# Performance work log

Hardware: AMD Instinct MI355X
Metric: run time of the kernel (lower is better)

## Reference

```python
import jax, jax.numpy as jnp
import numpy as np

N_ATOMS = 200000
AEV_DIM = 384
H1, H2, H3 = 160, 128, 96
N_SPECIES = 4
ALPHA = 0.1  # CELU alpha used by ANI atomic networks


def setup_inputs() -> dict:
    key = jax.random.key(0)
    ks = jax.random.split(key, 8)
    aev = jax.random.normal(ks[0], (N_ATOMS, AEV_DIM), dtype=jnp.float32)
    # Disjoint species partition (matches (species==s).nonzero() buffers)
    perm = jax.random.permutation(ks[1], N_ATOMS)
    chunk = N_ATOMS // N_SPECIES
    H_idx = perm[0 * chunk:1 * chunk]
    C_idx = perm[1 * chunk:2 * chunk]
    N_idx = perm[2 * chunk:3 * chunk]
    O_idx = perm[3 * chunk:4 * chunk]

    def init(k, shape, fan_in):
        return (jax.random.normal(k, shape, dtype=jnp.float32) / np.float32(np.sqrt(fan_in)))

    # Stacked per-species MLP params: leading axis = species (H,C,N,O)
    W1 = init(ks[2], (N_SPECIES, AEV_DIM, H1), AEV_DIM); b1 = jnp.zeros((N_SPECIES, H1), jnp.float32)
    W2 = init(ks[3], (N_SPECIES, H1, H2), H1);          b2 = jnp.zeros((N_SPECIES, H2), jnp.float32)
    W3 = init(ks[4], (N_SPECIES, H2, H3), H2);          b3 = jnp.zeros((N_SPECIES, H3), jnp.float32)
    W4 = init(ks[5], (N_SPECIES, H3, 1), H3);           b4 = jnp.zeros((N_SPECIES, 1), jnp.float32)
    return {"aev": aev,
            "W1": W1, "b1": b1, "W2": W2, "b2": b2,
            "W3": W3, "b3": b3, "W4": W4, "b4": b4,
            "H_idx": H_idx, "C_idx": C_idx, "N_idx": N_idx, "O_idx": O_idx}


def _species_mlp(x, W1, b1, W2, b2, W3, b3, W4, b4):
    h = jax.nn.celu(x @ W1 + b1, ALPHA)
    h = jax.nn.celu(h @ W2 + b2, ALPHA)
    h = jax.nn.celu(h @ W3 + b3, ALPHA)
    return (h @ W4 + b4).reshape(-1)  # per-atom scalar energy


def reference(aev, W1, b1, W2, b2, W3, b3, W4, b4, H_idx, C_idx, N_idx, O_idx):
    out = jnp.zeros((aev.shape[0],), dtype=aev.dtype)
    # Fixed small loop over the 4 species networks (structurally distinct experts)
    for s, idx in enumerate((H_idx, C_idx, N_idx, O_idx)):
        e = _species_mlp(aev[idx], W1[s], b1[s], W2[s], b2[s], W3[s], b3[s], W4[s], b4[s])
        out = out.at[idx].add(e)  # index_add_ scatter
    # output.unsqueeze(0).sum(dim=1) -> molecular energy, shape [1]
    return out[None, :].sum(axis=1)
```

## Files before the change

### kernel.cpp

```cpp
#include <hip/hip_runtime.h>

#define DI __device__ __forceinline__

constexpr int AEV = 384;
constexpr int H1N = 160;
constexpr int H2N = 128;
constexpr int H3N = 96;
constexpr int NSP = 4;
constexpr int W1P = 200;
constexpr int W2P = 168;
constexpr int W3P = 136;
constexpr int W3OFF = H2N * W2P;

using half8  = __attribute__((ext_vector_type(8))) _Float16;
using half4v = __attribute__((ext_vector_type(4))) _Float16;
using f32x4  = __attribute__((ext_vector_type(4))) float;

__device__ __align__(16) _Float16 g_w1[NSP * H1N * AEV];
__device__ __align__(16) _Float16 g_w2[NSP * H2N * H1N];
__device__ __align__(16) _Float16 g_w3[NSP * H3N * H2N];

DI float celu_f(float x) {
  return fmaxf(x, 0.f) + 0.1f * (exp2f(fminf(x, 0.f) * 14.426950408889634f) - 1.f);
}
DI f32x4 mfma16h(half8 a, half8 b, f32x4 c) {
  return __builtin_amdgcn_mfma_f32_16x16x32_f16(a, b, c, 0, 0, 0);
}
DI half8 cvt8(float4 a, float4 b) {
  half8 t;
  t[0] = (_Float16)a.x; t[1] = (_Float16)a.y; t[2] = (_Float16)a.z; t[3] = (_Float16)a.w;
  t[4] = (_Float16)b.x; t[5] = (_Float16)b.y; t[6] = (_Float16)b.z; t[7] = (_Float16)b.w;
  return t;
}
DI half4v shfl4(half4v v, int src) {
  union { half4v h; int i[2]; } u;
  u.h = v;
  u.i[0] = __shfl(u.i[0], src, 64);
  u.i[1] = __shfl(u.i[1], src, 64);
  return u.h;
}
DI half8 bfrag(const half4v* hb, int ks, int l15, int quad) {
  const int sLo = (quad & 1) * 32 + l15, sHi = sLo + 16;
  half4v loA = shfl4(hb[2 * ks], sLo),     loB = shfl4(hb[2 * ks + 1], sLo);
  half4v hiA = shfl4(hb[2 * ks], sHi),     hiB = shfl4(hb[2 * ks + 1], sHi);
  half4v lo = (quad & 2) ? loB : loA;
  half4v hi = (quad & 2) ? hiB : hiA;
  half8 b;
  b[0] = lo[0]; b[1] = lo[1]; b[2] = lo[2]; b[3] = lo[3];
  b[4] = hi[0]; b[5] = hi[1]; b[6] = hi[2]; b[7] = hi[3];
  return b;
}

template <int K, int N>
DI void tp(const float* __restrict__ src, _Float16* dst, int id) {
  constexpr int per = K * N;
  int s = id / per, r = id % per;
  int n = r / K, k = r % K;
  dst[s * per + n * K + k] = (_Float16)src[s * per + k * N + n];
}

__global__ void prep(const float* __restrict__ W1, const float* __restrict__ W2,
                     const float* __restrict__ W3, float* __restrict__ out) {
  int id = blockIdx.x * 256 + threadIdx.x;
  if (id == 0) out[0] = 0.f;
  constexpr int E1 = NSP * AEV * H1N;
  constexpr int E2 = NSP * H1N * H2N;
  constexpr int E3 = NSP * H2N * H3N;
  if (id < E1)                 tp<AEV, H1N>(W1, g_w1, id);
  else if (id < E1 + E2)       tp<H1N, H2N>(W2, g_w2, id - E1);
  else if (id < E1 + E2 + E3)  tp<H2N, H3N>(W3, g_w3, id - E1 - E2);
}

__global__ __launch_bounds__(512, 4) void fused_mlp(
    const float* __restrict__ aev,
    const float* __restrict__ b1, const float* __restrict__ b2,
    const float* __restrict__ b3,
    const float* __restrict__ W4, const float* __restrict__ pb4,
    const int* __restrict__ i0, const int* __restrict__ i1,
    const int* __restrict__ i2, const int* __restrict__ i3,
    int chunk, float* __restrict__ out) {
  __shared__ __align__(16) _Float16 WS[34560];
  __shared__ float RED[8];

  const int tid  = threadIdx.x;
  const int lane = tid & 63, wav = tid >> 6;
  const int l15  = lane & 15, quad = lane >> 4;
  const int s    = blockIdx.y;
  const int* idx = (s == 0) ? i0 : (s == 1) ? i1 : (s == 2) ? i2 : i3;

  const int a = blockIdx.x * 128 + wav * 16 + l15;
  const bool valid = (a < chunk);
  const int r = idx[valid ? a : (chunk - 1)];
  const float* xr = aev + (size_t)r * AEV + quad * 8;

  const _Float16* w1src = g_w1 + (size_t)s * H1N * AEV;

#pragma unroll
  for (int i = 0; i < 8; ++i) {
    int c = tid + i * 512;
    if (c < H1N * 24) {
      int n = c / 24, kc = c % 24;
      *(half8*)(WS + n * W1P + kc * 8) = *(const half8*)(w1src + n * AEV + kc * 8);
    }
  }
  __syncthreads();

  f32x4 acc[10];
#pragma unroll
  for (int m = 0; m < 10; ++m)
#pragma unroll
    for (int i = 0; i < 4; ++i) acc[m][i] = 0.f;

  float4 xf0 = *(const float4*)(xr), xf1 = *(const float4*)(xr + 4);
#pragma unroll
  for (int ks = 0; ks < 6; ++ks) {
    half8 bv = cvt8(xf0, xf1);
    xf0 = *(const float4*)(xr + (ks + 1) * 32);
    xf1 = *(const float4*)(xr + (ks + 1) * 32 + 4);
#pragma unroll
    for (int mt = 0; mt < 10; ++mt) {
      half8 aw = *(const half8*)(WS + (mt * 16 + l15) * W1P + ks * 32 + quad * 8);
      acc[mt] = mfma16h(aw, bv, acc[mt]);
    }
  }
  __syncthreads();
#pragma unroll
  for (int i = 0; i < 8; ++i) {
    int c = tid + i * 512;
    if (c < H1N * 24) {
      int n = c / 24, kc = c % 24;
      *(half8*)(WS + n * W1P + kc * 8) = *(const half8*)(w1src + 192 + n * AEV + kc * 8);
    }
  }
  __syncthreads();
#pragma unroll
  for (int ks = 6; ks < 12; ++ks) {
    half8 bv = cvt8(xf0, xf1);
    if (ks < 11) {
      xf0 = *(const float4*)(xr + (ks + 1) * 32);
      xf1 = *(const float4*)(xr + (ks + 1) * 32 + 4);
    }
#pragma unroll
    for (int mt = 0; mt < 10; ++mt) {
      half8 aw = *(const half8*)(WS + (mt * 16 + l15) * W1P + (ks - 6) * 32 + quad * 8);
      acc[mt] = mfma16h(aw, bv, acc[mt]);
    }
  }
  half4v hb[10];
#pragma unroll
  for (int mt = 0; mt < 10; ++mt) {
    float4 bb = *(const float4*)(b1 + s * H1N + mt * 16 + quad * 4);
    half4v o;
    o[0] = (_Float16)celu_f(acc[mt][0] + bb.x);
    o[1] = (_Float16)celu_f(acc[mt][1] + bb.y);
    o[2] = (_Float16)celu_f(acc[mt][2] + bb.z);
    o[3] = (_Float16)celu_f(acc[mt][3] + bb.w);
    hb[mt] = o;
  }

  __syncthreads();
  {
    const _Float16* w2src = g_w2 + (size_t)s * H2N * H1N;
    const _Float16* w3src = g_w3 + (size_t)s * H3N * H2N;
#pragma unroll
    for (int i = 0; i < 5; ++i) {
      int c = tid + i * 512;
      int n = c / 20, kc = c % 20;
      *(half8*)(WS + n * W2P + kc * 8) = *(const half8*)(w2src + n * H1N + kc * 8);
    }
#pragma unroll
    for (int i = 0; i < 3; ++i) {
      int c = tid + i * 512;
      int n = c / 16, kc = c % 16;
      *(half8*)(WS + W3OFF + n * W3P + kc * 8) = *(const half8*)(w3src + n * H2N + kc * 8);
    }
  }
  __syncthreads();

  f32x4 acc2[8];
#pragma unroll
  for (int m = 0; m < 8; ++m)
#pragma unroll
    for (int i = 0; i < 4; ++i) acc2[m][i] = 0.f;
#pragma unroll
  for (int ks = 0; ks < 5; ++ks) {
    half8 bv = bfrag(hb, ks, l15, quad);
#pragma unroll
    for (int mt = 0; mt < 8; ++mt) {
      half8 aw = *(const half8*)(WS + (mt * 16 + l15) * W2P + ks * 32 + quad * 8);
      acc2[mt] = mfma16h(aw, bv, acc2[mt]);
    }
  }
  half4v hb2[8];
#pragma unroll
  for (int mt = 0; mt < 8; ++mt) {
    float4 bb = *(const float4*)(b2 + s * H2N + mt * 16 + quad * 4);
    half4v o;
    o[0] = (_Float16)celu_f(acc2[mt][0] + bb.x);
    o[1] = (_Float16)celu_f(acc2[mt][1] + bb.y);
    o[2] = (_Float16)celu_f(acc2[mt][2] + bb.z);
    o[3] = (_Float16)celu_f(acc2[mt][3] + bb.w);
    hb2[mt] = o;
  }

  f32x4 acc3[6];
#pragma unroll
  for (int m = 0; m < 6; ++m)
#pragma unroll
    for (int i = 0; i < 4; ++i) acc3[m][i] = 0.f;
#pragma unroll
  for (int ks = 0; ks < 4; ++ks) {
    half8 bv = bfrag(hb2, ks, l15, quad);
#pragma unroll
    for (int mt = 0; mt < 6; ++mt) {
      half8 aw = *(const half8*)(WS + W3OFF + (mt * 16 + l15) * W3P + ks * 32 + quad * 8);
      acc3[mt] = mfma16h(aw, bv, acc3[mt]);
    }
  }

  float e = 0.f;
#pragma unroll
  for (int mt = 0; mt < 6; ++mt) {
    float4 bb = *(const float4*)(b3 + s * H3N + mt * 16 + quad * 4);
    float4 wv = *(const float4*)(W4 + s * H3N + mt * 16 + quad * 4);
    e += (float)(_Float16)celu_f(acc3[mt][0] + bb.x) * wv.x
       + (float)(_Float16)celu_f(acc3[mt][1] + bb.y) * wv.y
       + (float)(_Float16)celu_f(acc3[mt][2] + bb.z) * wv.z
       + (float)(_Float16)celu_f(acc3[mt][3] + bb.w) * wv.w;
  }
  e += __shfl_xor(e, 16, 64);
  e += __shfl_xor(e, 32, 64);
  e = (lane < 16 && valid) ? (e + pb4[s]) : 0.f;
#pragma unroll
  for (int off = 1; off < 64; off <<= 1) e += __shfl_xor(e, off, 64);
  if (lane == 0) RED[wav] = e;
  __syncthreads();
  if (tid == 0) {
    float t = 0.f;
#pragma unroll
    for (int i = 0; i < 8; ++i) t += RED[i];
    atomicAdd(out, t);
  }
}

extern "C" void kernel_launch(void* const* d_in, const int* in_sizes, int n_in,
                              void* d_out, int out_size, void* d_ws, size_t ws_size,
                              hipStream_t stream) {
  (void)n_in; (void)d_ws; (void)ws_size; (void)out_size;
  const float* aev = (const float*)d_in[0];
  const float* W1  = (const float*)d_in[1];
  const float* b1  = (const float*)d_in[2];
  const float* W2  = (const float*)d_in[3];
  const float* b2  = (const float*)d_in[4];
  const float* W3  = (const float*)d_in[5];
  const float* b3  = (const float*)d_in[6];
  const float* W4  = (const float*)d_in[7];
  const float* b4  = (const float*)d_in[8];
  const int* iH = (const int*)d_in[9];
  const int* iC = (const int*)d_in[10];
  const int* iN = (const int*)d_in[11];
  const int* iO = (const int*)d_in[12];
  const int chunk = in_sizes[9];

  constexpr int TOT = NSP * (AEV * H1N + H1N * H2N + H2N * H3N);
  prep<<<TOT / 256, 256, 0, stream>>>(W1, W2, W3, (float*)d_out);

  const int tiles = (chunk + 127) / 128;
  fused_mlp<<<dim3(tiles, NSP), 512, 0, stream>>>(aev, b1, b2, b3, W4, b4,
                                                  iH, iC, iN, iO, chunk, (float*)d_out);
}
```

Measured before the change: 478.1 us.

## Process two atom tiles per wave to reuse weight fragments across MFMAs

Halves the block to 256 threads (4 waves), with each wave now computing two 16-atom tiles. Every LDS weight fragment it loads feeds two MFMAs, which halves LDS weight reads per unit of work. The cost is double the accumulator registers per thread, lower occupancy (launch bounds 256,2), and fewer waves to cover global-load latency. The final reduction is simplified to match the new layout.

```diff
diff --git a/kernel.cpp b/kernel.cpp
--- a/kernel.cpp
+++ b/kernel.cpp
@@ -71,7 +71,7 @@
   else if (id < E1 + E2 + E3)  tp<H2N, H3N>(W3, g_w3, id - E1 - E2);
 }
 
-__global__ __launch_bounds__(512, 4) void fused_mlp(
+__global__ __launch_bounds__(256, 2) void fused_mlp(
     const float* __restrict__ aev,
     const float* __restrict__ b1, const float* __restrict__ b2,
     const float* __restrict__ b3,
@@ -80,7 +80,7 @@
     const int* __restrict__ i2, const int* __restrict__ i3,
     int chunk, float* __restrict__ out) {
   __shared__ __align__(16) _Float16 WS[34560];
-  __shared__ float RED[8];
+  __shared__ float RED[4];
 
   const int tid  = threadIdx.x;
   const int lane = tid & 63, wav = tid >> 6;
@@ -88,74 +88,86 @@
   const int s    = blockIdx.y;
   const int* idx = (s == 0) ? i0 : (s == 1) ? i1 : (s == 2) ? i2 : i3;
 
-  const int a = blockIdx.x * 128 + wav * 16 + l15;
-  const bool valid = (a < chunk);
-  const int r = idx[valid ? a : (chunk - 1)];
-  const float* xr = aev + (size_t)r * AEV + quad * 8;
+  const int a0 = blockIdx.x * 128 + wav * 32 + l15;
+  const int a1 = a0 + 16;
+  const bool v0 = (a0 < chunk), v1 = (a1 < chunk);
+  const int r0 = idx[v0 ? a0 : (chunk - 1)];
+  const int r1 = idx[v1 ? a1 : (chunk - 1)];
+  const float* xr0 = aev + (size_t)r0 * AEV + quad * 8;
+  const float* xr1 = aev + (size_t)r1 * AEV + quad * 8;
+  const float  b4s = pb4[s];
 
   const _Float16* w1src = g_w1 + (size_t)s * H1N * AEV;
 
 #pragma unroll
-  for (int i = 0; i < 8; ++i) {
-    int c = tid + i * 512;
-    if (c < H1N * 24) {
-      int n = c / 24, kc = c % 24;
-      *(half8*)(WS + n * W1P + kc * 8) = *(const half8*)(w1src + n * AEV + kc * 8);
-    }
-  }
-  __syncthreads();
-
-  f32x4 acc[10];
+  for (int i = 0; i < 15; ++i) {
+    int c = tid + i * 256;
+    int n = c / 24, kc = c % 24;
+    *(half8*)(WS + n * W1P + kc * 8) = *(const half8*)(w1src + n * AEV + kc * 8);
+  }
+  __syncthreads();
+
+  f32x4 acc[10][2];
 #pragma unroll
   for (int m = 0; m < 10; ++m)
 #pragma unroll
-    for (int i = 0; i < 4; ++i) acc[m][i] = 0.f;
-
-  float4 xf0 = *(const float4*)(xr), xf1 = *(const float4*)(xr + 4);
+    for (int nt = 0; nt < 2; ++nt)
+#pragma unroll
+      for (int i = 0; i < 4; ++i) acc[m][nt][i] = 0.f;
+
+  float4 p00 = *(const float4*)(xr0), p01 = *(const float4*)(xr0 + 4);
+  float4 p10 = *(const float4*)(xr1), p11 = *(const float4*)(xr1 + 4);
 #pragma unroll
   for (int ks = 0; ks < 6; ++ks) {
-    half8 bv = cvt8(xf0, xf1);
-    xf0 = *(const float4*)(xr + (ks + 1) * 32);
-    xf1 = *(const float4*)(xr + (ks + 1) * 32 + 4);
+    half8 bv0 = cvt8(p00, p01), bv1 = cvt8(p10, p11);
+    p00 = *(const float4*)(xr0 + (ks + 1) * 32);
+    p01 = *(const float4*)(xr0 + (ks + 1) * 32 + 4);
+    p10 = *(const float4*)(xr1 + (ks + 1) * 32);
+    p11 = *(const float4*)(xr1 + (ks + 1) * 32 + 4);
 #pragma unroll
     for (int mt = 0; mt < 10; ++mt) {
       half8 aw = *(const half8*)(WS + (mt * 16 + l15) * W1P + ks * 32 + quad * 8);
-      acc[mt] = mfma16h(aw, bv, acc[mt]);
-    }
-  }
-  __syncthreads();
-#pragma unroll
-  for (int i = 0; i < 8; ++i) {
-    int c = tid + i * 512;
-    if (c < H1N * 24) {
-      int n = c / 24, kc = c % 24;
-      *(half8*)(WS + n * W1P + kc * 8) = *(const half8*)(w1src + 192 + n * AEV + kc * 8);
-    }
+      acc[mt][0] = mfma16h(aw, bv0, acc[mt][0]);
+      acc[mt][1] = mfma16h(aw, bv1, acc[mt][1]);
+    }
+  }
+  __syncthreads();
+#pragma unroll
+  for (int i = 0; i < 15; ++i) {
+    int c = tid + i * 256;
+    int n = c / 24, kc = c % 24;
+    *(half8*)(WS + n * W1P + kc * 8) = *(const half8*)(w1src + 192 + n * AEV + kc * 8);
   }
   __syncthreads();
 #pragma unroll
   for (int ks = 6; ks < 12; ++ks) {
-    half8 bv = cvt8(xf0, xf1);
+    half8 bv0 = cvt8(p00, p01), bv1 = cvt8(p10, p11);
     if (ks < 11) {
-      xf0 = *(const float4*)(xr + (ks + 1) * 32);
-      xf1 = *(const float4*)(xr + (ks + 1) * 32 + 4);
+      p00 = *(const float4*)(xr0 + (ks + 1) * 32);
+      p01 = *(const float4*)(xr0 + (ks + 1) * 32 + 4);
+      p10 = *(const float4*)(xr1 + (ks + 1) * 32);
+      p11 = *(const float4*)(xr1 + (ks + 1) * 32 + 4);
     }
 #pragma unroll
     for (int mt = 0; mt < 10; ++mt) {
       half8 aw = *(const half8*)(WS + (mt * 16 + l15) * W1P + (ks - 6) * 32 + quad * 8);
-      acc[mt] = mfma16h(aw, bv, acc[mt]);
-    }
-  }
-  half4v hb[10];
+      acc[mt][0] = mfma16h(aw, bv0, acc[mt][0]);
+      acc[mt][1] = mfma16h(aw, bv1, acc[mt][1]);
+    }
+  }
+  half4v hb[2][10];
 #pragma unroll
   for (int mt = 0; mt < 10; ++mt) {
     float4 bb = *(const float4*)(b1 + s * H1N + mt * 16 + quad * 4);
-    half4v o;
-    o[0] = (_Float16)celu_f(acc[mt][0] + bb.x);
-    o[1] = (_Float16)celu_f(acc[mt][1] + bb.y);
-    o[2] = (_Float16)celu_f(acc[mt][2] + bb.z);
-    o[3] = (_Float16)celu_f(acc[mt][3] + bb.w);
-    hb[mt] = o;
+#pragma unroll
+    for (int nt = 0; nt < 2; ++nt) {
+      half4v o;
+      o[0] = (_Float16)celu_f(acc[mt][nt][0] + bb.x);
+      o[1] = (_Float16)celu_f(acc[mt][nt][1] + bb.y);
+      o[2] = (_Float16)celu_f(acc[mt][nt][2] + bb.z);
+      o[3] = (_Float16)celu_f(acc[mt][nt][3] + bb.w);
+      hb[nt][mt] = o;
+    }
   }
 
   __syncthreads();
@@ -163,84 +175,95 @@
     const _Float16* w2src = g_w2 + (size_t)s * H2N * H1N;
     const _Float16* w3src = g_w3 + (size_t)s * H3N * H2N;
 #pragma unroll
-    for (int i = 0; i < 5; ++i) {
-      int c = tid + i * 512;
+    for (int i = 0; i < 10; ++i) {
+      int c = tid + i * 256;
       int n = c / 20, kc = c % 20;
       *(half8*)(WS + n * W2P + kc * 8) = *(const half8*)(w2src + n * H1N + kc * 8);
     }
 #pragma unroll
-    for (int i = 0; i < 3; ++i) {
-      int c = tid + i * 512;
+    for (int i = 0; i < 6; ++i) {
+      int c = tid + i * 256;
       int n = c / 16, kc = c % 16;
       *(half8*)(WS + W3OFF + n * W3P + kc * 8) = *(const half8*)(w3src + n * H2N + kc * 8);
     }
   }
   __syncthreads();
 
-  f32x4 acc2[8];
+  f32x4 acc2[8][2];
 #pragma unroll
   for (int m = 0; m < 8; ++m)
 #pragma unroll
-    for (int i = 0; i < 4; ++i) acc2[m][i] = 0.f;
+    for (int nt = 0; nt < 2; ++nt)
+#pragma unroll
+      for (int i = 0; i < 4; ++i) acc2[m][nt][i] = 0.f;
 #pragma unroll
   for (int ks = 0; ks < 5; ++ks) {
-    half8 bv = bfrag(hb, ks, l15, quad);
+    half8 bv0 = bfrag(hb[0], ks, l15, quad);
+    half8 bv1 = bfrag(hb[1], ks, l15, quad);
 #pragma unroll
     for (int mt = 0; mt < 8; ++mt) {
       half8 aw = *(const half8*)(WS + (mt * 16 + l15) * W2P + ks * 32 + quad * 8);
-      acc2[mt] = mfma16h(aw, bv, acc2[mt]);
-    }
-  }
-  half4v hb2[8];
+      acc2[mt][0] = mfma16h(aw, bv0, acc2[mt][0]);
+      acc2[mt][1] = mfma16h(aw, bv1, acc2[mt][1]);
+    }
+  }
+  half4v hb2[2][8];
 #pragma unroll
   for (int mt = 0; mt < 8; ++mt) {
     float4 bb = *(const float4*)(b2 + s * H2N + mt * 16 + quad * 4);
-    half4v o;
-    o[0] = (_Float16)celu_f(acc2[mt][0] + bb.x);
-    o[1] = (_Float16)celu_f(acc2[mt][1] + bb.y);
-    o[2] = (_Float16)celu_f(acc2[mt][2] + bb.z);
-    o[3] = (_Float16)celu_f(acc2[mt][3] + bb.w);
-    hb2[mt] = o;
-  }
-
-  f32x4 acc3[6];
+#pragma unroll
+    for (int nt = 0; nt < 2; ++nt) {
+      half4v o;
+      o[0] = (_Float16)celu_f(acc2[mt][nt][0] + bb.x);
+      o[1] = (_Float16)celu_f(acc2[mt][nt][1] + bb.y);
+      o[2] = (_Float16)celu_f(acc2[mt][nt][2] + bb.z);
+      o[3] = (_Float16)celu_f(acc2[mt][nt][3] + bb.w);
+      hb2[nt][mt] = o;
+    }
+  }
+
+  f32x4 acc3[6][2];
 #pragma unroll
   for (int m = 0; m < 6; ++m)
 #pragma unroll
-    for (int i = 0; i < 4; ++i) acc3[m][i] = 0.f;
+    for (int nt = 0; nt < 2; ++nt)
+#pragma unroll
+      for (int i = 0; i < 4; ++i) acc3[m][nt][i] = 0.f;
 #pragma unroll
   for (int ks = 0; ks < 4; ++ks) {
-    half8 bv = bfrag(hb2, ks, l15, quad);
+    half8 bv0 = bfrag(hb2[0], ks, l15, quad);
+    half8 bv1 = bfrag(hb2[1], ks, l15, quad);
 #pragma unroll
     for (int mt = 0; mt < 6; ++mt) {
       half8 aw = *(const half8*)(WS + W3OFF + (mt * 16 + l15) * W3P + ks * 32 + quad * 8);
-      acc3[mt] = mfma16h(aw, bv, acc3[mt]);
-    }
-  }
-
-  float e = 0.f;
+      acc3[mt][0] = mfma16h(aw, bv0, acc3[mt][0]);
+      acc3[mt][1] = mfma16h(aw, bv1, acc3[mt][1]);
+    }
+  }
+
+  float e0 = 0.f, e1 = 0.f;
 #pragma unroll
   for (int mt = 0; mt < 6; ++mt) {
     float4 bb = *(const float4*)(b3 + s * H3N + mt * 16 + quad * 4);
     float4 wv = *(const float4*)(W4 + s * H3N + mt * 16 + quad * 4);
-    e += (float)(_Float16)celu_f(acc3[mt][0] + bb.x) * wv.x
-       + (float)(_Float16)celu_f(acc3[mt][1] + bb.y) * wv.y
-       + (float)(_Float16)celu_f(acc3[mt][2] + bb.z) * wv.z
-       + (float)(_Float16)celu_f(acc3[mt][3] + bb.w) * wv.w;
-  }
-  e += __shfl_xor(e, 16, 64);
-  e += __shfl_xor(e, 32, 64);
-  e = (lane < 16 && valid) ? (e + pb4[s]) : 0.f;
-#pragma unroll
-  for (int off = 1; off < 64; off <<= 1) e += __shfl_xor(e, off, 64);
-  if (lane == 0) RED[wav] = e;
-  __syncthreads();
-  if (tid == 0) {
-    float t = 0.f;
-#pragma unroll
-    for (int i = 0; i < 8; ++i) t += RED[i];
-    atomicAdd(out, t);
-  }
+    e0 += (float)(_Float16)celu_f(acc3[mt][0][0] + bb.x) * wv.x
+        + (float)(_Float16)celu_f(acc3[mt][0][1] + bb.y) * wv.y
+        + (float)(_Float16)celu_f(acc3[mt][0][2] + bb.z) * wv.z
+        + (float)(_Float16)celu_f(acc3[mt][0][3] + bb.w) * wv.w;
+    e1 += (float)(_Float16)celu_f(acc3[mt][1][0] + bb.x) * wv.x
+        + (float)(_Float16)celu_f(acc3[mt][1][1] + bb.y) * wv.y
+        + (float)(_Float16)celu_f(acc3[mt][1][2] + bb.z) * wv.z
+        + (float)(_Float16)celu_f(acc3[mt][1][3] + bb.w) * wv.w;
+  }
+  e0 += __shfl_xor(e0, 16, 64); e0 += __shfl_xor(e0, 32, 64);
+  e1 += __shfl_xor(e1, 16, 64); e1 += __shfl_xor(e1, 32, 64);
+  float tot = (v0 ? e0 + b4s : 0.f) + (v1 ? e1 + b4s : 0.f);
+  if (lane >= 16) tot = 0.f;
+#pragma unroll
+  for (int off = 1; off < 16; off <<= 1) tot += __shfl_xor(tot, off, 64);
+  if (lane == 0) RED[wav] = tot;
+  __syncthreads();
+  if (tid == 0) atomicAdd(out, RED[0] + RED[1] + RED[2] + RED[3]);
 }
 
 extern "C" void kernel_launch(void* const* d_in, const int* in_sizes, int n_in,
@@ -266,6 +289,6 @@
   prep<<<TOT / 256, 256, 0, stream>>>(W1, W2, W3, (float*)d_out);
 
   const int tiles = (chunk + 127) / 128;
-  fused_mlp<<<dim3(tiles, NSP), 512, 0, stream>>>(aev, b1, b2, b3, W4, b4,
+  fused_mlp<<<dim3(tiles, NSP), 256, 0, stream>>>(aev, b1, b2, b3, W4, b4,
                                                   iH, iC, iN, iO, chunk, (float*)d_out);
 }
```

After: 493.5 us. +3.2%, slower.
